# Kernel tuning notes

Measured on AMD Instinct MI355X. Metric: run time of the kernel, lower is better.

Reference implementation:

```python
import jax, jax.numpy as jnp
import numpy as np

CHUNK = 32
H = 4

def silu(x):
    return x * jax.nn.sigmoid(x)

def l2norm(x):
    return x * jax.lax.rsqrt(jnp.sum(x * x, -1, keepdims=True) + 1e-6)

def dwconv_causal(x_cl, w):
    # x_cl: (b, C, L), w: (C, k) depthwise causal conv (cross-correlation, left pad k-1)
    k = w.shape[1]
    xp = jnp.pad(x_cl, ((0, 0), (0, 0), (k - 1, 0)))
    return jax.lax.conv_general_dilated(xp, w[:, None, :], (1,), 'VALID',
        dimension_numbers=('NCH', 'OIH', 'NCH'), feature_group_count=x_cl.shape[1])

def short_conv_silu(x_bld, w):
    y = dwconv_causal(jnp.swapaxes(x_bld, 1, 2), w)
    return silu(jnp.swapaxes(y, 1, 2))

def delta_rule_chunkwise(q, k, v, beta, chunk=CHUNK):
    # q,k: (b,h,L,dk)  v: (b,h,L,dv)  beta: (b,h,L)
    b, h, L, dk = q.shape
    dv = v.shape[-1]
    pad = (-L) % chunk
    if pad:
        q, k, v = (jnp.pad(t, ((0, 0), (0, 0), (0, pad), (0, 0))) for t in (q, k, v))
        beta = jnp.pad(beta, ((0, 0), (0, 0), (0, pad)))
    n = (L + pad) // chunk
    q = l2norm(q)
    k = l2norm(k)
    v = v * beta[..., None]
    kb = k * beta[..., None]
    ch = lambda x: x.reshape(b, h, n, chunk, x.shape[-1])
    qc, kc, vc, kbc = map(ch, (q, k, v, kb))
    idx = jnp.arange(chunk)
    strict_lower = (idx[:, None] > idx[None, :]).astype(q.dtype)
    incl_lower = (idx[:, None] >= idx[None, :]).astype(q.dtype)
    # forward substitution to invert (I - tril(beta K K^T, -1)) per chunk
    attn = -jnp.einsum('bhncd,bhned->bhnce', kbc, kc) * strict_lower
    for i in range(1, chunk):
        upd = jnp.einsum('...j,...ji->...i', attn[..., i, :], attn[..., :, :i])
        attn = attn.at[..., i, :i].add(upd)
    attn = attn + jnp.eye(chunk, dtype=q.dtype)
    u = attn @ vc          # (b,h,n,c,dv)
    w = attn @ kbc         # (b,h,n,c,dk)
    xs = tuple(jnp.moveaxis(t, 2, 0) for t in (qc, kc, u, w))
    S0 = jnp.zeros((b, h, dk, dv), q.dtype)
    def step(S, x):
        qi, ki, ui, wi = x
        a_loc = jnp.einsum('bhcd,bhed->bhce', qi, ki) * incl_lower
        ui = ui - wi @ S
        oi = qi @ S + a_loc @ ui
        S = S + jnp.einsum('bhcd,bhcv->bhdv', ki, ui)
        return S, oi
    S, o = jax.lax.scan(step, S0, xs)
    o = jnp.moveaxis(o, 0, 2).reshape(b, h, n * chunk, dv)[:, :, :L]
    return o, S

def multiscale_conv(v, ms_w3, ms_w15, ms_w31, kernel_mix_w, channel_mixer_w):
    # v: (b,l,h,d)
    b, l, h, d = v.shape
    x = jnp.swapaxes(v.reshape(b, l, h * d), 1, 2)  # (b, h*d, l)
    outs = [dwconv_causal(x, w) for w in (ms_w3, ms_w15, ms_w31)]
    y = jnp.concatenate(outs, axis=1)               # (b, 3*h*d, l)
    # faithful to torch rearrange 'b (h kd) l -> b l h kd' on the concat layout
    y = y.reshape(b, h, 3 * d, l).transpose(0, 3, 1, 2)  # (b,l,h,3d)
    y = y @ kernel_mix_w                            # (b,l,h,d)
    y = (y.reshape(b, l, h * d) @ channel_mixer_w).reshape(b, l, h, d)
    return y

def _forward(hidden_states, Wq, Wk, Wv, Wb, conv_q_w, conv_k_w, conv_v_w,
             ms_w3, ms_w15, ms_w31, kernel_mix_w, channel_mixer_w,
             fusion_w1, fusion_b1, fusion_w2, fusion_b2, o_norm_w, Wo):
    b, L, D = hidden_states.shape
    h = H
    dk = Wq.shape[1] // h
    dv = Wv.shape[1] // h
    q = short_conv_silu(hidden_states @ Wq, conv_q_w).reshape(b, L, h, dk)
    k = short_conv_silu(hidden_states @ Wk, conv_k_w).reshape(b, L, h, dk)
    v = short_conv_silu(hidden_states @ Wv, conv_v_w).reshape(b, L, h, dv)
    v_direct = v
    beta = jax.nn.sigmoid(hidden_states @ Wb)  # (b,L,h)
    tr = lambda x: jnp.swapaxes(x, 1, 2)
    delta_out, _S = delta_rule_chunkwise(tr(q), tr(k), tr(v), tr(beta))
    delta_out = jnp.swapaxes(delta_out, 1, 2)  # (b,L,h,dv)
    ms_out = multiscale_conv(v_direct, ms_w3, ms_w15, ms_w31, kernel_mix_w, channel_mixer_w)
    bn = lambda x: jnp.mean(jnp.abs(x), -1)    # (b,L,h)
    gate_features = jnp.concatenate([hidden_states, bn(ms_out), bn(delta_out), bn(v_direct)], -1)
    hdn = jax.nn.gelu(gate_features @ fusion_w1 + fusion_b1, approximate=False)
    logits = (hdn @ fusion_w2 + fusion_b2).reshape(b, L, h, 3)
    wts = jax.nn.softmax(logits, -1)
    o = wts[..., 0:1] * ms_out + wts[..., 1:2] * delta_out + wts[..., 2:3] * v_direct
    o = o * jax.lax.rsqrt(jnp.mean(o * o, -1, keepdims=True) + 1e-5) * o_norm_w  # RMSNorm
    return o.reshape(b, L, h * dv) @ Wo

def setup_inputs() -> dict:
    B, L, D = 4, 2048, 1024
    h, d = H, D // H
    key = jax.random.key(0)
    ks = jax.random.split(key, 20)
    nrm = lambda k, shp, s: (jax.random.normal(k, shp, dtype=jnp.float32) * s)
    inp = {
        'hidden_states': nrm(ks[0], (B, L, D), 1.0),
        'Wq': nrm(ks[1], (D, D), D ** -0.5),
        'Wk': nrm(ks[2], (D, D), D ** -0.5),
        'Wv': nrm(ks[3], (D, D), D ** -0.5),
        'Wb': nrm(ks[4], (D, h), D ** -0.5),
        'conv_q_w': nrm(ks[5], (D, 4), 0.3),
        'conv_k_w': nrm(ks[6], (D, 4), 0.3),
        'conv_v_w': nrm(ks[7], (D, 4), 0.3),
        'ms_w3': nrm(ks[8], (D, 3), 0.02),
        'ms_w15': nrm(ks[9], (D, 15), 0.02),
        'ms_w31': nrm(ks[10], (D, 31), 0.02),
        'kernel_mix_w': nrm(ks[11], (3 * d, d), (3 * d) ** -0.5),
        'channel_mixer_w': nrm(ks[12], (D, D), D ** -0.5),
        'fusion_w1': nrm(ks[13], (D + 3 * h, 2 * D), (D + 3 * h) ** -0.5),
        'fusion_b1': jnp.zeros((2 * D,), jnp.float32),
        'fusion_w2': nrm(ks[14], (2 * D, 3 * h), (2 * D) ** -0.5),
        'fusion_b2': jnp.concatenate([jnp.zeros((2 * h,), jnp.float32), jnp.ones((h,), jnp.float32)]),
        'o_norm_w': jnp.ones((d,), jnp.float32),
        'Wo': nrm(ks[15], (D, D), D ** -0.5),
    }
    return inp

def reference(hidden_states, Wq, Wk, Wv, Wb, conv_q_w, conv_k_w, conv_v_w,
              ms_w3, ms_w15, ms_w31, kernel_mix_w, channel_mixer_w,
              fusion_w1, fusion_b1, fusion_w2, fusion_b2, o_norm_w, Wo):
    return _forward(hidden_states, Wq, Wk, Wv, Wb, conv_q_w, conv_k_w, conv_v_w,
                    ms_w3, ms_w15, ms_w31, kernel_mix_w, channel_mixer_w,
                    fusion_w1, fusion_b1, fusion_w2, fusion_b2, o_norm_w, Wo)
```

## Files before the change

kernel.cpp:

```cpp
#include <hip/hip_runtime.h>
#include <math.h>


typedef __attribute__((ext_vector_type(8))) __bf16 bf16x8;
typedef __attribute__((ext_vector_type(4))) float f32x4;

__device__ inline ushort f2bf(float f) {
    union { float f; unsigned u; } x; x.f = f;
    unsigned u = x.u;
    u += 0x7fffu + ((u >> 16) & 1u);
    return (ushort)(u >> 16);
}
__device__ inline float bf2f(ushort h) {
    union { unsigned u; float f; } x; x.u = ((unsigned)h) << 16;
    return x.f;
}
__device__ inline float ldf(float v) { return v; }
__device__ inline float ldf(ushort v) { return bf2f(v); }

template<int EPI>
__global__ __launch_bounds__(256) void gemm_mfma(
    const ushort* __restrict__ A, const ushort* __restrict__ BT,
    const float* __restrict__ bias, const float* __restrict__ extA,
    const float* __restrict__ extB, void* __restrict__ Cout,
    int M, int N, int K)
{
    __shared__ ushort As[2][128 * 32];
    __shared__ ushort Bs[2][128 * 32];
    __shared__ float bns[(EPI >= 2) ? 128 * 13 : 1];
    __shared__ float exb[(EPI >= 2) ? 12 * 128 : 1];
    const int tid = threadIdx.x;
    const int row0 = blockIdx.y * 128, col0 = blockIdx.x * 128;
    const int lane = tid & 63, wave = tid >> 6;
    const int wr = (wave >> 1) * 64, wc = (wave & 1) * 64;

    if (EPI >= 2) {
        for (int e = tid; e < 128 * 12; e += 256)
            bns[(e / 12) * 13 + (e % 12)] = extA[(long)(row0 + e / 12) * 12 + e % 12];
        for (int e = tid; e < 12 * 128; e += 256)
            exb[e] = extB[(long)(e >> 7) * N + col0 + (e & 127)];
    }

    f32x4 acc[4][4];
    #pragma unroll
    for (int m = 0; m < 4; ++m)
        #pragma unroll
        for (int n = 0; n < 4; ++n) {
            acc[m][n][0] = 0.f; acc[m][n][1] = 0.f;
            acc[m][n][2] = 0.f; acc[m][n][3] = 0.f;
        }

    const int rA = lane & 15;
    const int ko = (lane >> 4) * 8;
    const int srow = tid >> 2;
    const int skk = (tid & 3) * 8;

    for (int k0 = 0; k0 < K; k0 += 64) {
        #pragma unroll
        for (int hf = 0; hf < 2; ++hf) {
            #pragma unroll
            for (int i = 0; i < 2; ++i) {
                const long ga = (long)(row0 + i * 64 + srow) * K + k0 + hf * 32 + skk;
                __builtin_amdgcn_global_load_lds(
                    (const __attribute__((address_space(1))) void*)(A + ga),
                    (__attribute__((address_space(3))) void*)(&As[hf][0] + i * 2048 + wave * 512),
                    16, 0, 0);
                const long gb = (long)(col0 + i * 64 + srow) * K + k0 + hf * 32 + skk;
                __builtin_amdgcn_global_load_lds(
                    (const __attribute__((address_space(1))) void*)(BT + gb),
                    (__attribute__((address_space(3))) void*)(&Bs[hf][0] + i * 2048 + wave * 512),
                    16, 0, 0);
            }
        }
        __syncthreads();
        #pragma unroll
        for (int hf = 0; hf < 2; ++hf) {
            bf16x8 af[4], bfr[4];
            #pragma unroll
            for (int m = 0; m < 4; ++m)
                af[m] = *(const bf16x8*)(&As[hf][0] + (wr + m * 16 + rA) * 32 + ko);
            #pragma unroll
            for (int n = 0; n < 4; ++n)
                bfr[n] = *(const bf16x8*)(&Bs[hf][0] + (wc + n * 16 + rA) * 32 + ko);
            #pragma unroll
            for (int m = 0; m < 4; ++m)
                #pragma unroll
                for (int n = 0; n < 4; ++n)
                    acc[m][n] = __builtin_amdgcn_mfma_f32_16x16x32_bf16(af[m], bfr[n], acc[m][n], 0, 0, 0);
        }
        __syncthreads();
    }

    const int crow = (lane >> 4) * 4;
    const int ccol = lane & 15;
    #pragma unroll
    for (int m = 0; m < 4; ++m) {
        #pragma unroll
        for (int n = 0; n < 4; ++n) {
            #pragma unroll
            for (int r = 0; r < 4; ++r) {
                const int rl = wr + m * 16 + crow + r;
                const int cl = wc + n * 16 + ccol;
                float vv = acc[m][n][r];
                if (EPI >= 2) {
                    vv += bias[col0 + cl];
                    #pragma unroll
                    for (int j = 0; j < 12; ++j) vv += bns[rl * 13 + j] * exb[j * 128 + cl];
                    vv = 0.5f * vv * (1.f + erff(vv * 0.70710678118654752f));
                }
                const long off = (long)(row0 + rl) * N + col0 + cl;
                if (EPI == 0) ((float*)Cout)[off] = vv;
                else ((ushort*)Cout)[off] = f2bf(vv);
            }
        }
    }
}

__global__ __launch_bounds__(256) void transpose_cast(const float* __restrict__ W,
    ushort* __restrict__ WT, int K, int N)
{
    __shared__ float t[32][33];
    const int k0 = blockIdx.y * 32, n0 = blockIdx.x * 32;
    const int c = threadIdx.x & 31, r8 = threadIdx.x >> 5;
    #pragma unroll
    for (int rr = 0; rr < 4; ++rr) {
        const int r = r8 + rr * 8;
        t[r][c] = W[(long)(k0 + r) * N + n0 + c];
    }
    __syncthreads();
    #pragma unroll
    for (int rr = 0; rr < 4; ++rr) {
        const int r = r8 + rr * 8;
        WT[(long)(n0 + r) * K + k0 + c] = f2bf(t[c][r]);
    }
}

__global__ __launch_bounds__(256) void cast_bf16(const float* __restrict__ x,
    ushort* __restrict__ y)
{
    const long i = ((long)blockIdx.x * 256 + threadIdx.x) * 4;
    const float4 v = *(const float4*)(x + i);
    ushort4 o;
    o.x = f2bf(v.x); o.y = f2bf(v.y); o.z = f2bf(v.z); o.w = f2bf(v.w);
    *(ushort4*)(y + i) = o;
}

template<int NOUT, int MODE, typename TA>
__global__ __launch_bounds__(256) void gemm_smallN(const TA* __restrict__ A,
    const float* __restrict__ Bm, const float* __restrict__ bias,
    float* __restrict__ Cm, int K)
{
    __shared__ float part[4][NOUT];
    __shared__ float sm[NOUT];
    const int m = blockIdx.x, tid = threadIdx.x;
    const TA* ar = A + (long)m * K;
    float acc[NOUT];
    #pragma unroll
    for (int j = 0; j < NOUT; ++j) acc[j] = 0.f;
    for (int k = tid; k < K; k += 256) {
        const float a = ldf(ar[k]);
        #pragma unroll
        for (int j = 0; j < NOUT; ++j) acc[j] += a * Bm[(long)k * NOUT + j];
    }
    #pragma unroll
    for (int j = 0; j < NOUT; ++j)
        for (int off = 32; off > 0; off >>= 1) acc[j] += __shfl_down(acc[j], off);
    const int wid = tid >> 6, lane = tid & 63;
    if (lane == 0) {
        #pragma unroll
        for (int j = 0; j < NOUT; ++j) part[wid][j] = acc[j];
    }
    __syncthreads();
    if (tid < NOUT) {
        float s = part[0][tid] + part[1][tid] + part[2][tid] + part[3][tid];
        if (MODE == 0) {
            Cm[(long)m * NOUT + tid] = 1.f / (1.f + expf(-s));
        } else {
            sm[tid] = s + bias[tid];
        }
    }
    if (MODE == 1) {
        __syncthreads();
        if (tid < NOUT) {
            const int hh = tid / 3, r = tid - hh * 3;
            const float a0 = sm[hh * 3], a1 = sm[hh * 3 + 1], a2 = sm[hh * 3 + 2];
            const float mx = fmaxf(a0, fmaxf(a1, a2));
            const float e0 = expf(a0 - mx), e1 = expf(a1 - mx), e2 = expf(a2 - mx);
            const float mine = (r == 0) ? e0 : ((r == 1) ? e1 : e2);
            Cm[(long)m * NOUT + tid] = mine / (e0 + e1 + e2);
        }
    }
}

__global__ __launch_bounds__(256) void conv4_silu(const float* __restrict__ x,
    const float* __restrict__ wc, float* __restrict__ y)
{
    const long idx = (long)blockIdx.x * 256 + threadIdx.x;
    const int c = (int)(idx & 1023);
    const long bl = idx >> 10;
    const int l = (int)(bl & 2047);
    const long b = bl >> 11;
    const float* xp = x + b * 2048 * 1024 + c;
    const float* wp = wc + c * 4;
    float s = 0.f;
    #pragma unroll
    for (int t = 0; t < 4; ++t) {
        const int ll = l - 3 + t;
        if (ll >= 0) s += xp[(long)ll * 1024] * wp[t];
    }
    y[idx] = s / (1.f + expf(-s));
}

__global__ __launch_bounds__(256) void l2norm_bf16(const float* __restrict__ x,
    ushort* __restrict__ y)
{
    const long wid = ((long)blockIdx.x * 256 + threadIdx.x) >> 6;
    const int lane = threadIdx.x & 63;
    const float4 xv = *(const float4*)(x + wid * 256 + lane * 4);
    float ss = xv.x * xv.x + xv.y * xv.y + xv.z * xv.z + xv.w * xv.w;
    for (int off = 32; off > 0; off >>= 1) ss += __shfl_down(ss, off);
    ss = __shfl(ss, 0);
    const float inv = rsqrtf(ss + 1e-6f);
    ushort4 o;
    o.x = f2bf(xv.x * inv); o.y = f2bf(xv.y * inv);
    o.z = f2bf(xv.z * inv); o.w = f2bf(xv.w * inv);
    *(ushort4*)(y + wid * 256 + lane * 4) = o;
}

__global__ __launch_bounds__(256) void chunk_prep(
    const ushort* __restrict__ qn, const ushort* __restrict__ kn,
    const float* __restrict__ v, const float* __restrict__ beta,
    float* __restrict__ u, ushort* __restrict__ w16,
    ushort* __restrict__ kT16, ushort* __restrict__ al16)
{
    __shared__ __align__(16) ushort kn16[32 * 264];
    __shared__ __align__(16) ushort kb16[32 * 264];
    __shared__ __align__(16) float  vb[32 * 260];
    __shared__ float Ms[32 * 33];
    __shared__ float Rs[32 * 33];
    __shared__ float bet[32];
    const int blk = blockIdx.x;
    const int n = blk & 63;
    const int bh = blk >> 6;
    const int h = bh & 3;
    const int b = bh >> 2;
    const int tid = threadIdx.x;
    const long lbase = (long)b * 2048 + n * 32;

    if (tid < 32) bet[tid] = beta[(lbase + tid) * 4 + h];
    __syncthreads();

    #pragma unroll
    for (int it = 0; it < 4; ++it) {
        const int e2 = tid + it * 256;
        const int c = e2 >> 5, d8 = (e2 & 31) * 8;
        const uint4 kv = *(const uint4*)(kn + (lbase + c) * 1024 + h * 256 + d8);
        *(uint4*)&kn16[c * 264 + d8] = kv;
        const float bc = bet[c];
        uint4 kb;
        kb.x = (uint)f2bf(bf2f((ushort)(kv.x & 0xffffu)) * bc) |
               ((uint)f2bf(bf2f((ushort)(kv.x >> 16)) * bc) << 16);
        kb.y = (uint)f2bf(bf2f((ushort)(kv.y & 0xffffu)) * bc) |
               ((uint)f2bf(bf2f((ushort)(kv.y >> 16)) * bc) << 16);
        kb.z = (uint)f2bf(bf2f((ushort)(kv.z & 0xffffu)) * bc) |
               ((uint)f2bf(bf2f((ushort)(kv.z >> 16)) * bc) << 16);
        kb.w = (uint)f2bf(bf2f((ushort)(kv.w & 0xffffu)) * bc) |
               ((uint)f2bf(bf2f((ushort)(kv.w >> 16)) * bc) << 16);
        *(uint4*)&kb16[c * 264 + d8] = kb;
    }
    #pragma unroll
    for (int it = 0; it < 8; ++it) {
        const int e2 = tid + it * 256;
        const int c = e2 >> 6, d4 = (e2 & 63) * 4;
        float4 vv = *(const float4*)(v + (lbase + c) * 1024 + h * 256 + d4);
        const float bc = bet[c];
        vv.x *= bc; vv.y *= bc; vv.z *= bc; vv.w *= bc;
        *(float4*)&vb[c * 260 + d4] = vv;
    }
    __syncthreads();

    for (int e = tid; e < 8192; e += 256)
        kT16[(long)blk * 8192 + e] = kn16[(e & 31) * 264 + (e >> 5)];

    const int lane = tid & 63, wave = tid >> 6;
    const int wr2 = (wave >> 1) * 16, wc2 = (wave & 1) * 16;
    const int rA = lane & 15, ko = (lane >> 4) * 8;
    {
        f32x4 accM, accA;
        accM[0] = 0.f; accM[1] = 0.f; accM[2] = 0.f; accM[3] = 0.f;
        accA[0] = 0.f; accA[1] = 0.f; accA[2] = 0.f; accA[3] = 0.f;
        const ushort* qrow = qn + (lbase + wr2 + rA) * 1024 + h * 256 + ko;
        #pragma unroll
        for (int ks = 0; ks < 8; ++ks) {
            const bf16x8 bfK = *(const bf16x8*)&kn16[(wc2 + rA) * 264 + ks * 32 + ko];
            const bf16x8 afM = *(const bf16x8*)&kb16[(wr2 + rA) * 264 + ks * 32 + ko];
            accM = __builtin_amdgcn_mfma_f32_16x16x32_bf16(afM, bfK, accM, 0, 0, 0);
            const bf16x8 afQ = *(const bf16x8*)(qrow + ks * 32);
            accA = __builtin_amdgcn_mfma_f32_16x16x32_bf16(afQ, bfK, accA, 0, 0, 0);
        }
        const int ccol = lane & 15, crow = (lane >> 4) * 4;
        #pragma unroll
        for (int r = 0; r < 4; ++r) {
            const int i = wr2 + crow + r, j = wc2 + ccol;
            const float mv = (i > j) ? -accM[r] : 0.f;
            Ms[i * 33 + j] = mv;
            Rs[i * 33 + j] = mv + ((i == j) ? 1.f : 0.f);
            al16[(long)blk * 1024 + i * 32 + j] = f2bf((i >= j) ? accA[r] : 0.f);
        }
    }
    __syncthreads();

    const int j = tid & 31, i0 = tid >> 5;
    for (int it = 0; it < 4; ++it) {
        float p4[4] = {0.f, 0.f, 0.f, 0.f};
        for (int kk = 0; kk < 32; ++kk) {
            const float pb = Ms[kk * 33 + j];
            #pragma unroll
            for (int ii = 0; ii < 4; ++ii) p4[ii] += Ms[(i0 + 8 * ii) * 33 + kk] * pb;
        }
        __syncthreads();
        #pragma unroll
        for (int ii = 0; ii < 4; ++ii) Ms[(i0 + 8 * ii) * 33 + j] = p4[ii];
        __syncthreads();
        float r4[4] = {0.f, 0.f, 0.f, 0.f};
        for (int kk = 0; kk < 32; ++kk) {
            const float pb = Ms[kk * 33 + j];
            #pragma unroll
            for (int ii = 0; ii < 4; ++ii) r4[ii] += Rs[(i0 + 8 * ii) * 33 + kk] * pb;
        }
        __syncthreads();
        #pragma unroll
        for (int ii = 0; ii < 4; ++ii) Rs[(i0 + 8 * ii) * 33 + j] += r4[ii];
        __syncthreads();
    }

    {
        const int dd = tid;
        float accU[32], accW[32];
        #pragma unroll
        for (int r = 0; r < 32; ++r) { accU[r] = 0.f; accW[r] = 0.f; }
        for (int kk = 0; kk < 32; ++kk) {
            const float vv = vb[kk * 260 + dd];
            const float bb = bf2f(kb16[kk * 264 + dd]);
            #pragma unroll
            for (int r = 0; r < 32; ++r) {
                const float rr = Rs[r * 33 + kk];
                accU[r] += rr * vv;
                accW[r] += rr * bb;
            }
        }
        const long base = (long)blk * 32;
        #pragma unroll
        for (int r = 0; r < 32; ++r) {
            u  [(base + r) * 256 + dd] = accU[r];
            w16[(base + r) * 256 + dd] = f2bf(accW[r]);
        }
    }
}

__global__ __launch_bounds__(64, 1) void delta_scan_mfma(
    const ushort* __restrict__ q16, const ushort* __restrict__ kT16,
    const ushort* __restrict__ w16, const float* __restrict__ u,
    const ushort* __restrict__ al16, float* __restrict__ dt)
{
    __shared__ __align__(16) ushort Sb[16 * 264];
    __shared__ __align__(16) ushort Ub[16 * 40];
    const int blk = blockIdx.x;
    const int bh = blk & 15;
    const int sl = blk >> 4;
    const int h = bh & 3;
    const int b = bh >> 2;
    const int v0 = sl * 16;
    const int lane = threadIdx.x;
    const int col = lane & 15;
    const int grp = lane >> 4;

    const ushort* wp  = w16  + ((long)bh * 64 * 32 + col) * 256 + grp * 8;
    const ushort* qp  = q16  + ((long)b * 2048 + col) * 1024 + h * 256 + grp * 8;
    const ushort* kp  = kT16 + ((long)bh * 64 * 256 + col) * 32 + grp * 8;
    const ushort* ap  = al16 + ((long)bh * 64 * 32 + col) * 32 + grp * 8;
    const float*  Ug  = u    + ((long)bh * 64 * 32 + grp * 4) * 256 + v0 + col;
    float*        dp  = dt   + ((long)b * 2048 + grp * 4) * 1024 + h * 256 + v0 + col;

    f32x4 S[16];
    #pragma unroll
    for (int t = 0; t < 16; ++t) { S[t][0] = 0.f; S[t][1] = 0.f; S[t][2] = 0.f; S[t][3] = 0.f; }

    bf16x8 wf[2][8], qf[2][8], kf[16], alf[2], sf[8];
    float upre[8];

    #pragma unroll
    for (int kb = 0; kb < 8; ++kb)
        #pragma unroll
        for (int e = 0; e < 8; ++e) sf[kb][e] = (__bf16)0.f;

    #pragma unroll
    for (int rt = 0; rt < 2; ++rt)
        #pragma unroll
        for (int kb = 0; kb < 8; ++kb) {
            wf[rt][kb] = *(const bf16x8*)(wp + rt * 4096 + kb * 32);
            qf[rt][kb] = *(const bf16x8*)(qp + (long)rt * 16384 + kb * 32);
        }
    #pragma unroll
    for (int t = 0; t < 16; ++t) kf[t] = *(const bf16x8*)(kp + t * 512);
    alf[0] = *(const bf16x8*)(ap);
    alf[1] = *(const bf16x8*)(ap + 512);
    #pragma unroll
    for (int rt = 0; rt < 2; ++rt)
        #pragma unroll
        for (int r = 0; r < 4; ++r)
            upre[rt * 4 + r] = Ug[rt * 4096 + r * 256];

    for (int n = 0; n < 64; ++n) {
        f32x4 up[2];
        #pragma unroll
        for (int rt = 0; rt < 2; ++rt) {
            f32x4 a; a[0] = 0.f; a[1] = 0.f; a[2] = 0.f; a[3] = 0.f;
            #pragma unroll
            for (int kb = 0; kb < 8; ++kb)
                a = __builtin_amdgcn_mfma_f32_16x16x32_bf16(wf[rt][kb], sf[kb], a, 0, 0, 0);
            #pragma unroll
            for (int r = 0; r < 4; ++r)
                up[rt][r] = upre[rt * 4 + r] - a[r];
        }
        if (n < 63) {
            #pragma unroll
            for (int rt = 0; rt < 2; ++rt)
                #pragma unroll
                for (int kb = 0; kb < 8; ++kb)
                    wf[rt][kb] = *(const bf16x8*)(wp + (long)(n + 1) * 8192 + rt * 4096 + kb * 32);
        }

        #pragma unroll
        for (int rt = 0; rt < 2; ++rt) {
            ushort4 p;
            p.x = f2bf(up[rt][0]); p.y = f2bf(up[rt][1]);
            p.z = f2bf(up[rt][2]); p.w = f2bf(up[rt][3]);
            *(ushort4*)&Ub[col * 40 + rt * 16 + grp * 4] = p;
        }
        const bf16x8 uf = *(const bf16x8*)&Ub[col * 40 + grp * 8];

        #pragma unroll
        for (int rt = 0; rt < 2; ++rt) {
            f32x4 a; a[0] = 0.f; a[1] = 0.f; a[2] = 0.f; a[3] = 0.f;
            #pragma unroll
            for (int kb = 0; kb < 8; ++kb)
                a = __builtin_amdgcn_mfma_f32_16x16x32_bf16(qf[rt][kb], sf[kb], a, 0, 0, 0);
            a = __builtin_amdgcn_mfma_f32_16x16x32_bf16(alf[rt], uf, a, 0, 0, 0);
            #pragma unroll
            for (int r = 0; r < 4; ++r)
                dp[(long)n * 32768 + rt * 16384 + r * 1024] = a[r];
        }
        if (n < 63) {
            #pragma unroll
            for (int rt = 0; rt < 2; ++rt)
                #pragma unroll
                for (int kb = 0; kb < 8; ++kb)
                    qf[rt][kb] = *(const bf16x8*)(qp + (long)(n + 1) * 32768 + (long)rt * 16384 + kb * 32);
            alf[0] = *(const bf16x8*)(ap + (long)(n + 1) * 1024);
            alf[1] = *(const bf16x8*)(ap + (long)(n + 1) * 1024 + 512);
        }

        #pragma unroll
        for (int t = 0; t < 16; ++t)
            S[t] = __builtin_amdgcn_mfma_f32_16x16x32_bf16(kf[t], uf, S[t], 0, 0, 0);
        if (n < 63) {
            #pragma unroll
            for (int t = 0; t < 16; ++t)
                kf[t] = *(const bf16x8*)(kp + (long)(n + 1) * 8192 + t * 512);
            #pragma unroll
            for (int rt = 0; rt < 2; ++rt)
                #pragma unroll
                for (int r = 0; r < 4; ++r)
                    upre[rt * 4 + r] = Ug[(long)(n + 1) * 8192 + rt * 4096 + r * 256];
        }

        #pragma unroll
        for (int t = 0; t < 16; ++t) {
            ushort4 p;
            p.x = f2bf(S[t][0]); p.y = f2bf(S[t][1]);
            p.z = f2bf(S[t][2]); p.w = f2bf(S[t][3]);
            *(ushort4*)&Sb[col * 264 + t * 16 + grp * 4] = p;
        }
        #pragma unroll
        for (int kb = 0; kb < 8; ++kb)
            sf[kb] = *(const bf16x8*)&Sb[col * 264 + kb * 32 + grp * 8];
    }
}

__global__ __launch_bounds__(256) void ms_conv(const float* __restrict__ v,
    const float* __restrict__ w3, const float* __restrict__ w15,
    const float* __restrict__ w31, ushort* __restrict__ y)
{
    const int bid = blockIdx.x;
    const int b = bid >> 10;
    const int oct = (bid >> 2) & 255;
    const int c = ((bid & 3) << 8) + threadIdx.x;
    const int l0 = oct << 3;
    const float* vb = v + ((long)b * 2048) * 1024 + c;
    ushort* yb = y + ((long)b * 2048) * 3072 + c;

    float win[38];
    #pragma unroll
    for (int t = 0; t < 38; ++t) {
        const int ll = l0 - 30 + t;
        win[t] = (ll >= 0) ? vb[(long)ll * 1024] : 0.f;
    }
    {
        float W[31];
        #pragma unroll
        for (int t = 0; t < 31; ++t) W[t] = w31[c * 31 + t];
        #pragma unroll
        for (int j = 0; j < 8; ++j) {
            float s = 0.f;
            #pragma unroll
            for (int t = 0; t < 31; ++t) s += win[j + t] * W[t];
            yb[(long)(l0 + j) * 3072 + 2048] = f2bf(s);
        }
    }
    {
        float W[15];
        #pragma unroll
        for (int t = 0; t < 15; ++t) W[t] = w15[c * 15 + t];
        #pragma unroll
        for (int j = 0; j < 8; ++j) {
            float s = 0.f;
            #pragma unroll
            for (int t = 0; t < 15; ++t) s += win[j + 16 + t] * W[t];
            yb[(long)(l0 + j) * 3072 + 1024] = f2bf(s);
        }
    }
    {
        float W[3];
        #pragma unroll
        for (int t = 0; t < 3; ++t) W[t] = w3[c * 3 + t];
        #pragma unroll
        for (int j = 0; j < 8; ++j) {
            float s = 0.f;
            #pragma unroll
            for (int t = 0; t < 3; ++t) s += win[j + 28 + t] * W[t];
            yb[(long)(l0 + j) * 3072] = f2bf(s);
        }
    }
}

__global__ __launch_bounds__(256) void build_bn(const float* __restrict__ ms,
    const float* __restrict__ dt, const float* __restrict__ v,
    float* __restrict__ bn)
{
    const int bl = blockIdx.x, tid = threadIdx.x;
    const long rb = (long)bl * 1024;
    const int wid = tid >> 6, lane = tid & 63;
    const long base = rb + wid * 256 + lane * 4;
    float* g = bn + (long)bl * 12;
    float4 a;
    float s;
    a = *(const float4*)(ms + base);
    s = fabsf(a.x) + fabsf(a.y) + fabsf(a.z) + fabsf(a.w);
    for (int off = 32; off > 0; off >>= 1) s += __shfl_down(s, off);
    if (lane == 0) g[wid] = s * (1.f / 256.f);
    a = *(const float4*)(dt + base);
    s = fabsf(a.x) + fabsf(a.y) + fabsf(a.z) + fabsf(a.w);
    for (int off = 32; off > 0; off >>= 1) s += __shfl_down(s, off);
    if (lane == 0) g[4 + wid] = s * (1.f / 256.f);
    a = *(const float4*)(v + base);
    s = fabsf(a.x) + fabsf(a.y) + fabsf(a.z) + fabsf(a.w);
    for (int off = 32; off > 0; off >>= 1) s += __shfl_down(s, off);
    if (lane == 0) g[8 + wid] = s * (1.f / 256.f);
}

__global__ __launch_bounds__(256) void blend_rms(const float* __restrict__ ms,
    const float* __restrict__ dt, const float* __restrict__ v,
    const float* __restrict__ wts, const float* __restrict__ onw,
    ushort* __restrict__ o)
{
    const int bl = blockIdx.x, tid = threadIdx.x;
    const int wid = tid >> 6, lane = tid & 63;
    const long base = (long)bl * 1024 + wid * 256 + lane * 4;
    const float* wr = wts + (long)bl * 12 + wid * 3;
    const float w0 = wr[0], w1 = wr[1], w2 = wr[2];
    const float4 m = *(const float4*)(ms + base);
    const float4 d = *(const float4*)(dt + base);
    const float4 x = *(const float4*)(v + base);
    float4 ov;
    ov.x = w0 * m.x + w1 * d.x + w2 * x.x;
    ov.y = w0 * m.y + w1 * d.y + w2 * x.y;
    ov.z = w0 * m.z + w1 * d.z + w2 * x.z;
    ov.w = w0 * m.w + w1 * d.w + w2 * x.w;
    float ss = ov.x * ov.x + ov.y * ov.y + ov.z * ov.z + ov.w * ov.w;
    for (int off = 32; off > 0; off >>= 1) ss += __shfl_down(ss, off);
    ss = __shfl(ss, 0);
    const float inv = rsqrtf(ss * (1.f / 256.f) + 1e-5f);
    const float4 nw = *(const float4*)(onw + lane * 4);
    ushort4 ob;
    ob.x = f2bf(ov.x * inv * nw.x); ob.y = f2bf(ov.y * inv * nw.y);
    ob.z = f2bf(ov.z * inv * nw.z); ob.w = f2bf(ov.w * inv * nw.w);
    *(ushort4*)(o + base) = ob;
}

extern "C" void kernel_launch(void* const* d_in, const int* in_sizes, int n_in,
                              void* d_out, int out_size, void* d_ws, size_t ws_size,
                              hipStream_t stream)
{
    (void)in_sizes; (void)n_in; (void)out_size; (void)ws_size;
    const float* hid   = (const float*)d_in[0];
    const float* Wq    = (const float*)d_in[1];
    const float* Wk    = (const float*)d_in[2];
    const float* Wv    = (const float*)d_in[3];
    const float* Wb    = (const float*)d_in[4];
    const float* cq    = (const float*)d_in[5];
    const float* ck    = (const float*)d_in[6];
    const float* cv    = (const float*)d_in[7];
    const float* w3    = (const float*)d_in[8];
    const float* w15   = (const float*)d_in[9];
    const float* w31   = (const float*)d_in[10];
    const float* kmix  = (const float*)d_in[11];
    const float* cmix  = (const float*)d_in[12];
    const float* fw1   = (const float*)d_in[13];
    const float* fb1   = (const float*)d_in[14];
    const float* fw2   = (const float*)d_in[15];
    const float* fb2   = (const float*)d_in[16];
    const float* onw   = (const float*)d_in[17];
    const float* Wo    = (const float*)d_in[18];
    float* out = (float*)d_out;

    const size_t MiB = 1024 * 1024;
    char* W = (char*)d_ws;
    float*  s0    = (float*)(W);
    char*   s1c   = W + 32 * MiB;
    float*  s1    = (float*)s1c;
    float*  s2    = (float*)(W + 64 * MiB);
    char*   s3    = W + 96 * MiB;
    float*  s4    = (float*)(W + 128 * MiB);
    ushort* hid16 = (ushort*)(W + 160 * MiB);
    ushort* WqT   = (ushort*)(W + 176 * MiB);
    ushort* WkT   = WqT   + 1024 * 1024;
    ushort* WvT   = WkT   + 1024 * 1024;
    ushort* cmixT = WvT   + 1024 * 1024;
    ushort* WoT   = cmixT + 1024 * 1024;
    ushort* fw1T  = WoT   + 1024 * 1024;
    ushort* kmixT = fw1T  + 2048 * 1024;
    float*  beta  = (float*)(W + 191 * MiB);
    ushort* al16  = (ushort*)(W + 191 * MiB + 128 * 1024);
    float*  bnf   = (float*)(W + 193 * MiB + 128 * 1024);
    float*  wts   = bnf + 98304;

    ushort* q16    = (ushort*)s3;
    ushort* k16    = (ushort*)(s3 + 16 * MiB);
    ushort* mix16  = q16;
    ushort* ofin16 = k16;
    ushort* yms16  = (ushort*)s0;
    ushort* hdn16  = (ushort*)s0;
    float*  qlin = s0; float* qtmp = s1;
    float*  u = s0;
    ushort* w16  = (ushort*)s1c;
    ushort* kT16 = (ushort*)(s1c + 16 * MiB);
    float*  dt = s2; float* v = s4; float* msout = s1;

    const dim3 T256(256);
    cast_bf16<<<8192, T256, 0, stream>>>(hid, hid16);
    transpose_cast<<<dim3(32, 32), T256, 0, stream>>>(Wq, WqT, 1024, 1024);
    transpose_cast<<<dim3(32, 32), T256, 0, stream>>>(Wk, WkT, 1024, 1024);
    transpose_cast<<<dim3(32, 32), T256, 0, stream>>>(Wv, WvT, 1024, 1024);
    transpose_cast<<<dim3(32, 32), T256, 0, stream>>>(cmix, cmixT, 1024, 1024);
    transpose_cast<<<dim3(32, 32), T256, 0, stream>>>(Wo, WoT, 1024, 1024);
    transpose_cast<<<dim3(64, 32), T256, 0, stream>>>(fw1, fw1T, 1024, 2048);
    transpose_cast<<<dim3(8, 24), T256, 0, stream>>>(kmix, kmixT, 768, 256);
    gemm_mfma<0><<<dim3(8, 64), T256, 0, stream>>>(hid16, WqT, nullptr, nullptr, nullptr, qlin, 8192, 1024, 1024);
    conv4_silu<<<32768, T256, 0, stream>>>(qlin, cq, qtmp);
    l2norm_bf16<<<8192, T256, 0, stream>>>(qtmp, q16);
    gemm_mfma<0><<<dim3(8, 64), T256, 0, stream>>>(hid16, WkT, nullptr, nullptr, nullptr, qlin, 8192, 1024, 1024);
    conv4_silu<<<32768, T256, 0, stream>>>(qlin, ck, qtmp);
    l2norm_bf16<<<8192, T256, 0, stream>>>(qtmp, k16);
    gemm_mfma<0><<<dim3(8, 64), T256, 0, stream>>>(hid16, WvT, nullptr, nullptr, nullptr, qlin, 8192, 1024, 1024);
    conv4_silu<<<32768, T256, 0, stream>>>(qlin, cv, v);
    gemm_smallN<4, 0><<<8192, T256, 0, stream>>>(hid, Wb, nullptr, beta, 1024);
    chunk_prep<<<1024, T256, 0, stream>>>(q16, k16, v, beta, u, w16, kT16, al16);
    delta_scan_mfma<<<256, dim3(64), 0, stream>>>(q16, kT16, w16, u, al16, dt);
    ms_conv<<<4096, T256, 0, stream>>>(v, w3, w15, w31, yms16);
    gemm_mfma<1><<<dim3(2, 256), T256, 0, stream>>>(yms16, kmixT, nullptr, nullptr, nullptr, mix16, 32768, 256, 768);
    gemm_mfma<0><<<dim3(8, 64), T256, 0, stream>>>(mix16, cmixT, nullptr, nullptr, nullptr, msout, 8192, 1024, 1024);
    build_bn<<<8192, T256, 0, stream>>>(msout, dt, v, bnf);
    gemm_mfma<3><<<dim3(16, 64), T256, 0, stream>>>(hid16, fw1T, fb1, bnf, fw1 + 1024L * 2048, hdn16, 8192, 2048, 1024);
    gemm_smallN<12, 1><<<8192, T256, 0, stream>>>(hdn16, fw2, fb2, wts, 2048);
    blend_rms<<<8192, T256, 0, stream>>>(msout, dt, v, wts, onw, ofin16);
    gemm_mfma<0><<<dim3(8, 64), T256, 0, stream>>>(ofin16, WoT, nullptr, nullptr, nullptr, out, 8192, 1024, 1024);
}
```

Baseline: 722.0 us.

## Fuse conv+SiLU with l2norm for q/k and pack delta scan into 8-wave blocks

The q and k paths now use one kernel that does the causal depthwise conv, SiLU and per-head L2 normalization. This removes an fp32 intermediate round trip and one launch per path. The delta-rule scan now runs 8 value-slices as 8 waves in one 512-thread block, with per-wave LDS buffers, instead of 256 single-wave blocks. The intent is to share the CU's L2/L1 for the common w/q/k loads across slices. The catch is that only 32 blocks run, so fewer CUs are busy in the latency-bound scan.

```diff
diff --git a/kernel.cpp b/kernel.cpp
--- a/kernel.cpp
+++ b/kernel.cpp
@@ -211,20 +211,36 @@
     y[idx] = s / (1.f + expf(-s));
 }
 
-__global__ __launch_bounds__(256) void l2norm_bf16(const float* __restrict__ x,
-    ushort* __restrict__ y)
-{
-    const long wid = ((long)blockIdx.x * 256 + threadIdx.x) >> 6;
-    const int lane = threadIdx.x & 63;
-    const float4 xv = *(const float4*)(x + wid * 256 + lane * 4);
-    float ss = xv.x * xv.x + xv.y * xv.y + xv.z * xv.z + xv.w * xv.w;
+__global__ __launch_bounds__(256) void conv4_silu_l2norm(const float* __restrict__ x,
+    const float* __restrict__ wc, ushort* __restrict__ y)
+{
+    const int bl = blockIdx.x, tid = threadIdx.x;
+    const int l = bl & 2047;
+    const long b = bl >> 11;
+    const int c0 = tid * 4;
+    const float* xp = x + (b * 2048 + l) * 1024 + c0;
+    float s[4] = {0.f, 0.f, 0.f, 0.f};
+    #pragma unroll
+    for (int t = 0; t < 4; ++t) {
+        const int ll = l - 3 + t;
+        if (ll >= 0) {
+            const float4 xv = *(const float4*)(xp + (long)(ll - l) * 1024);
+            s[0] += xv.x * wc[(c0 + 0) * 4 + t];
+            s[1] += xv.y * wc[(c0 + 1) * 4 + t];
+            s[2] += xv.z * wc[(c0 + 2) * 4 + t];
+            s[3] += xv.w * wc[(c0 + 3) * 4 + t];
+        }
+    }
+    #pragma unroll
+    for (int i = 0; i < 4; ++i) s[i] = s[i] / (1.f + expf(-s[i]));
+    float ss = s[0] * s[0] + s[1] * s[1] + s[2] * s[2] + s[3] * s[3];
     for (int off = 32; off > 0; off >>= 1) ss += __shfl_down(ss, off);
     ss = __shfl(ss, 0);
     const float inv = rsqrtf(ss + 1e-6f);
     ushort4 o;
-    o.x = f2bf(xv.x * inv); o.y = f2bf(xv.y * inv);
-    o.z = f2bf(xv.z * inv); o.w = f2bf(xv.w * inv);
-    *(ushort4*)(y + wid * 256 + lane * 4) = o;
+    o.x = f2bf(s[0] * inv); o.y = f2bf(s[1] * inv);
+    o.z = f2bf(s[2] * inv); o.w = f2bf(s[3] * inv);
+    *(ushort4*)(y + (long)bl * 1024 + c0) = o;
 }
 
 __global__ __launch_bounds__(256) void chunk_prep(
@@ -358,20 +374,23 @@
     }
 }
 
-__global__ __launch_bounds__(64, 1) void delta_scan_mfma(
+__global__ __launch_bounds__(512, 2) void delta_scan_mfma(
     const ushort* __restrict__ q16, const ushort* __restrict__ kT16,
     const ushort* __restrict__ w16, const float* __restrict__ u,
     const ushort* __restrict__ al16, float* __restrict__ dt)
 {
-    __shared__ __align__(16) ushort Sb[16 * 264];
-    __shared__ __align__(16) ushort Ub[16 * 40];
+    __shared__ __align__(16) ushort Sb[8][16 * 264];
+    __shared__ __align__(16) ushort Ub[8][16 * 40];
     const int blk = blockIdx.x;
     const int bh = blk & 15;
-    const int sl = blk >> 4;
+    const int half = blk >> 4;
+    const int tid = threadIdx.x;
+    const int wv = tid >> 6;
+    const int lane = tid & 63;
+    const int sl = half * 8 + wv;
     const int h = bh & 3;
     const int b = bh >> 2;
     const int v0 = sl * 16;
-    const int lane = threadIdx.x;
     const int col = lane & 15;
     const int grp = lane >> 4;
 
@@ -436,9 +455,9 @@
             ushort4 p;
             p.x = f2bf(up[rt][0]); p.y = f2bf(up[rt][1]);
             p.z = f2bf(up[rt][2]); p.w = f2bf(up[rt][3]);
-            *(ushort4*)&Ub[col * 40 + rt * 16 + grp * 4] = p;
-        }
-        const bf16x8 uf = *(const bf16x8*)&Ub[col * 40 + grp * 8];
+            *(ushort4*)&Ub[wv][col * 40 + rt * 16 + grp * 4] = p;
+        }
+        const bf16x8 uf = *(const bf16x8*)&Ub[wv][col * 40 + grp * 8];
 
         #pragma unroll
         for (int rt = 0; rt < 2; ++rt) {
@@ -480,11 +499,11 @@
             ushort4 p;
             p.x = f2bf(S[t][0]); p.y = f2bf(S[t][1]);
             p.z = f2bf(S[t][2]); p.w = f2bf(S[t][3]);
-            *(ushort4*)&Sb[col * 264 + t * 16 + grp * 4] = p;
+            *(ushort4*)&Sb[wv][col * 264 + t * 16 + grp * 4] = p;
         }
         #pragma unroll
         for (int kb = 0; kb < 8; ++kb)
-            sf[kb] = *(const bf16x8*)&Sb[col * 264 + kb * 32 + grp * 8];
+            sf[kb] = *(const bf16x8*)&Sb[wv][col * 264 + kb * 32 + grp * 8];
     }
 }
 
@@ -651,7 +670,7 @@
     ushort* ofin16 = k16;
     ushort* yms16  = (ushort*)s0;
     ushort* hdn16  = (ushort*)s0;
-    float*  qlin = s0; float* qtmp = s1;
+    float*  qlin = s0;
     float*  u = s0;
     ushort* w16  = (ushort*)s1c;
     ushort* kT16 = (ushort*)(s1c + 16 * MiB);
@@ -667,16 +686,14 @@
     transpose_cast<<<dim3(64, 32), T256, 0, stream>>>(fw1, fw1T, 1024, 2048);
     transpose_cast<<<dim3(8, 24), T256, 0, stream>>>(kmix, kmixT, 768, 256);
     gemm_mfma<0><<<dim3(8, 64), T256, 0, stream>>>(hid16, WqT, nullptr, nullptr, nullptr, qlin, 8192, 1024, 1024);
-    conv4_silu<<<32768, T256, 0, stream>>>(qlin, cq, qtmp);
-    l2norm_bf16<<<8192, T256, 0, stream>>>(qtmp, q16);
+    conv4_silu_l2norm<<<8192, T256, 0, stream>>>(qlin, cq, q16);
     gemm_mfma<0><<<dim3(8, 64), T256, 0, stream>>>(hid16, WkT, nullptr, nullptr, nullptr, qlin, 8192, 1024, 1024);
-    conv4_silu<<<32768, T256, 0, stream>>>(qlin, ck, qtmp);
-    l2norm_bf16<<<8192, T256, 0, stream>>>(qtmp, k16);
+    conv4_silu_l2norm<<<8192, T256, 0, stream>>>(qlin, ck, k16);
     gemm_mfma<0><<<dim3(8, 64), T256, 0, stream>>>(hid16, WvT, nullptr, nullptr, nullptr, qlin, 8192, 1024, 1024);
     conv4_silu<<<32768, T256, 0, stream>>>(qlin, cv, v);
     gemm_smallN<4, 0><<<8192, T256, 0, stream>>>(hid, Wb, nullptr, beta, 1024);
     chunk_prep<<<1024, T256, 0, stream>>>(q16, k16, v, beta, u, w16, kT16, al16);
-    delta_scan_mfma<<<256, dim3(64), 0, stream>>>(q16, kT16, w16, u, al16, dt);
+    delta_scan_mfma<<<32, dim3(512), 0, stream>>>(q16, kT16, w16, u, al16, dt);
     ms_conv<<<4096, T256, 0, stream>>>(v, w3, w15, w31, yms16);
     gemm_mfma<1><<<dim3(2, 256), T256, 0, stream>>>(yms16, kmixT, nullptr, nullptr, nullptr, mix16, 32768, 256, 768);
     gemm_mfma<0><<<dim3(8, 64), T256, 0, stream>>>(mix16, cmixT, nullptr, nullptr, nullptr, msout, 8192, 1024, 1024);
```

Measured after the change: 1.597 ms. 2.21x slower.
